# Kernel optimization log

Hardware: AMD Instinct MI355X
Metric: run time of the kernel (lower is better)

## Reference

```python
import jax, jax.numpy as jnp
import numpy as np

N_NODES = 50000
N_EDGES = 1_600_000
D = 128


def setup_inputs() -> dict:
    key = jax.random.key(0)
    k1, k2, k3 = jax.random.split(key, 3)
    x = jax.random.normal(k1, (N_NODES, D), dtype=jnp.float32)
    edge_index = jax.random.randint(k2, (2, N_EDGES), 0, N_NODES, dtype=jnp.int64)
    W = jax.random.normal(k3, (D, D), dtype=jnp.float32) / np.sqrt(D)
    b = jnp.zeros((D,), dtype=jnp.float32)
    return {"x": x, "edge_index": edge_index, "W": W, "b": b}


def _sgconv(x, src, dst, W, b, n):
    # gcn_norm with self-loops: D^{-1/2} (A + I) D^{-1/2}
    loop = jnp.arange(n, dtype=src.dtype)
    src = jnp.concatenate([src, loop])
    dst = jnp.concatenate([dst, loop])
    ones = jnp.ones(src.shape[0], dtype=x.dtype)
    deg = jax.ops.segment_sum(ones, dst, num_segments=n)  # in-degree incl. self-loop
    dinv = jnp.where(deg > 0, jax.lax.rsqrt(deg), jnp.zeros_like(deg))
    norm = dinv[src] * dinv[dst]                      # [E+N]
    msg = x[src] * norm[:, None]                      # gather + scale, [E+N, D]
    agg = jax.ops.segment_sum(msg, dst, num_segments=n)  # scatter-add, [N, D]
    return agg @ W.T + b                              # SGConv linear (K=1)


def reference(x, edge_index, W, b):
    n = x.shape[0]
    h = _sgconv(x, edge_index[0], edge_index[1], W, b, n)
    return x + jax.nn.relu(h)
```

## Files before the change

kernel.cpp:

```cpp
#include <hip/hip_runtime.h>
#include <hip/hip_fp16.h>

#define D 128
#define BSHIFT 6
#define BSIZE 64
#define NBMAX 1024
#define BCAP 3072
#define PREP_BLOCKS 256
#define OVF_CAP 65536
#define GB_THREADS 1024

using half8 = __attribute__((ext_vector_type(8))) _Float16;
using float4v = __attribute__((ext_vector_type(4))) float;
using floatx2 = __attribute__((ext_vector_type(2))) float;

__global__ __launch_bounds__(256) void prep_kernel(const int* __restrict__ src,
                                                   const int* __restrict__ dst,
                                                   int* __restrict__ bucket_cnt,
                                                   int* __restrict__ pairs,
                                                   int* __restrict__ ovfA_cnt,
                                                   int2* __restrict__ ovfA,
                                                   int E, int NB) {
    __shared__ int sbase[NBMAX];
    __shared__ int cur[NBMAX];
    const int t = threadIdx.x;
    for (int b = t; b < NB; b += 256) { sbase[b] = 0; cur[b] = 0; }
    __syncthreads();

    int chunk = (((E + (int)gridDim.x - 1) / (int)gridDim.x) + 3) & ~3;
    int start = blockIdx.x * chunk;
    int end = min(start + chunk, E);

    for (int i = start + 4 * t; i < end; i += 4 * 256) {
        if (i + 3 < end) {
            int4 v = *(const int4*)&dst[i];
            atomicAdd(&sbase[v.x >> BSHIFT], 1);
            atomicAdd(&sbase[v.y >> BSHIFT], 1);
            atomicAdd(&sbase[v.z >> BSHIFT], 1);
            atomicAdd(&sbase[v.w >> BSHIFT], 1);
        } else {
            for (int j = i; j < end; ++j) atomicAdd(&sbase[dst[j] >> BSHIFT], 1);
        }
    }
    __syncthreads();

    for (int b = t; b < NB; b += 256) {
        int h = sbase[b];
        sbase[b] = h ? atomicAdd(&bucket_cnt[b], h) : 0;
    }
    __syncthreads();

    auto place = [&](int dd, int ss) {
        int b = dd >> BSHIFT;
        int p = sbase[b] + atomicAdd(&cur[b], 1);
        if (p < BCAP) {
            pairs[(size_t)b * BCAP + p] = (ss << BSHIFT) | (dd & (BSIZE - 1));
        } else {
            int q = atomicAdd(ovfA_cnt, 1);
            if (q < OVF_CAP) ovfA[q] = make_int2(dd, ss);
        }
    };

    for (int i = start + 4 * t; i < end; i += 4 * 256) {
        if (i + 3 < end) {
            int4 dv = *(const int4*)&dst[i];
            int4 sv = *(const int4*)&src[i];
            place(dv.x, sv.x);
            place(dv.y, sv.y);
            place(dv.z, sv.z);
            place(dv.w, sv.w);
        } else {
            for (int j = i; j < end; ++j) place(dst[j], src[j]);
        }
    }
}

__global__ __launch_bounds__(256) void xw_kernel(const float* __restrict__ x,
                                                 const float* __restrict__ W,
                                                 const int* __restrict__ pairs,
                                                 const int* __restrict__ bucket_cnt,
                                                 const int* __restrict__ ovfA_cnt,
                                                 const int2* __restrict__ ovfA,
                                                 unsigned char* __restrict__ xw, int N) {
    __shared__ _Float16 Bf[128 * 128];
    __shared__ int degX[BSIZE];
    const int t = threadIdx.x;
    const int b = blockIdx.x;
    if (t < BSIZE) degX[t] = 0;
    __syncthreads();

    {
        int cnt = min(bucket_cnt[b], BCAP);
        const int* pp = pairs + (size_t)b * BCAP;
        for (int i = t; i < cnt; i += 256) atomicAdd(&degX[pp[i] & (BSIZE - 1)], 1);
        int na = *ovfA_cnt;
        if (na > 0) {
            if (na > OVF_CAP) na = OVF_CAP;
            for (int k = t; k < na; k += 256) {
                int dd = ovfA[k].x;
                if ((dd >> BSHIFT) == b) atomicAdd(&degX[dd & (BSIZE - 1)], 1);
            }
        }
    }

    {
        int n = t >> 1;
        int jt = n >> 4, nlo = n & 15;
        int kbase = (t & 1) * 64;
#pragma unroll
        for (int o = 0; o < 8; ++o) {
            int k0 = kbase + o * 8;
            float4 f0 = *(const float4*)&W[n * 128 + k0];
            float4 f1 = *(const float4*)&W[n * 128 + k0 + 4];
            int kt = k0 >> 5, quad = (k0 >> 3) & 3;
            half8 h;
            h[0] = (_Float16)f0.x; h[1] = (_Float16)f0.y;
            h[2] = (_Float16)f0.z; h[3] = (_Float16)f0.w;
            h[4] = (_Float16)f1.x; h[5] = (_Float16)f1.y;
            h[6] = (_Float16)f1.z; h[7] = (_Float16)f1.w;
            *(half8*)&Bf[(size_t)(((kt * 8 + jt) * 4 + quad) * 16 + nlo) * 8] = h;
        }
    }
    __syncthreads();

    const int wave = t >> 6, lane = t & 63;
    const int quad = lane >> 4, nlo = lane & 15;
    const int r0 = b * 64 + wave * 16;
    const int rA = r0 + nlo;
    const int rAc = (rA < N) ? rA : (N - 1);
    const float dv = rsqrtf((float)degX[rAc - b * 64] + 1.0f);

    float4v acc[8];
#pragma unroll
    for (int j = 0; j < 8; ++j) acc[j] = (float4v){0.f, 0.f, 0.f, 0.f};

#pragma unroll
    for (int kt = 0; kt < 4; ++kt) {
        const float* xp = x + (size_t)rAc * D + kt * 32 + quad * 8;
        float4 a0 = *(const float4*)xp;
        float4 a1 = *(const float4*)(xp + 4);
        half8 va;
        va[0] = (_Float16)(a0.x * dv); va[1] = (_Float16)(a0.y * dv);
        va[2] = (_Float16)(a0.z * dv); va[3] = (_Float16)(a0.w * dv);
        va[4] = (_Float16)(a1.x * dv); va[5] = (_Float16)(a1.y * dv);
        va[6] = (_Float16)(a1.z * dv); va[7] = (_Float16)(a1.w * dv);
#pragma unroll
        for (int jt = 0; jt < 8; ++jt) {
            half8 vb = *(half8*)&Bf[(size_t)((kt * 8 + jt) * 64 + lane) * 8];
            acc[jt] = __builtin_amdgcn_mfma_f32_16x16x32_f16(va, vb, acc[jt], 0, 0, 0);
        }
    }

#pragma unroll
    for (int reg = 0; reg < 4; ++reg) {
        int row = r0 + quad * 4 + reg;
        if (row < N) {
            int u0 = __builtin_amdgcn_cvt_pk_fp8_f32(acc[0][reg], acc[1][reg], 0, false);
            u0 = __builtin_amdgcn_cvt_pk_fp8_f32(acc[2][reg], acc[3][reg], u0, true);
            int u1 = __builtin_amdgcn_cvt_pk_fp8_f32(acc[4][reg], acc[5][reg], 0, false);
            u1 = __builtin_amdgcn_cvt_pk_fp8_f32(acc[6][reg], acc[7][reg], u1, true);
            *(uint2*)(xw + (size_t)row * 128 + nlo * 8) = make_uint2((unsigned)u0, (unsigned)u1);
        }
    }
}

__global__ __launch_bounds__(GB_THREADS) void gatherB_kernel(
    const float* __restrict__ x, const unsigned char* __restrict__ xw,
    const int* __restrict__ pairs, const int* __restrict__ bucket_cnt,
    const float* __restrict__ bias, const int* __restrict__ ovfA_cnt,
    const int2* __restrict__ ovfA, float* __restrict__ out, int N) {
    __shared__ int lds_src[BCAP];
    __shared__ int degL[BSIZE], offs[BSIZE], cur[BSIZE], spillc[BSIZE];
    const int b = blockIdx.x;
    const int t = threadIdx.x;
    if (t < BSIZE) { degL[t] = 0; cur[t] = 0; spillc[t] = 0; }
    __syncthreads();
    const int cnt = min(bucket_cnt[b], BCAP);
    int na = *ovfA_cnt;
    if (na > OVF_CAP) na = OVF_CAP;

    int my_w[3], my_n = 0;
    for (int i = t; i < cnt; i += GB_THREADS) {
        int w = pairs[(size_t)b * BCAP + i];
        my_w[my_n++] = w;
        atomicAdd(&degL[w & (BSIZE - 1)], 1);
    }
    if (na > 0) {
        for (int k = t; k < na; k += GB_THREADS) {
            int dd = ovfA[k].x;
            if ((dd >> BSHIFT) == b) atomicAdd(&spillc[dd & (BSIZE - 1)], 1);
        }
    }
    __syncthreads();

    if (t < BSIZE) {
        int v = degL[t];
        int s = v;
#pragma unroll
        for (int o = 1; o < 64; o <<= 1) {
            int u = __shfl_up(s, o, 64);
            if (t >= o) s += u;
        }
        offs[t] = s - v;
    }
    __syncthreads();

    for (int k = 0; k < my_n; ++k) {
        int w = my_w[k];
        int dl = w & (BSIZE - 1);
        int p = atomicAdd(&cur[dl], 1);
        lds_src[offs[dl] + p] = w >> BSHIFT;
    }
    __syncthreads();

    const int wave = t >> 6, lane = t & 63;
    const int half = lane >> 5, c31 = lane & 31;
    const unsigned int* xw32 = (const unsigned int*)xw;

    int col[4];
    float bcol[4];
#pragma unroll
    for (int k = 0; k < 4; ++k) {
        int s = 4 * c31 + k;
        col[k] = ((s & 7) << 4) + (s >> 3);
        bcol[k] = bias[col[k]];
    }

    for (int q = 0; q < 4; ++q) {
        int dl = wave * 4 + q;
        int node = b * BSIZE + dl;
        if (node >= N) break;
        int start = offs[dl];
        int end = start + degL[dl];
        float dvd = rsqrtf((float)(degL[dl] + spillc[dl]) + 1.0f);
        size_t noff = (size_t)node * D;

        float a0 = 0.f, a1 = 0.f, a2 = 0.f, a3 = 0.f;

        int e = start;
        for (; e + 7 < end; e += 8) {
            int r0 = lds_src[e + 0 + half], r1 = lds_src[e + 2 + half];
            int r2 = lds_src[e + 4 + half], r3 = lds_src[e + 6 + half];
            unsigned int w0 = xw32[(size_t)r0 * 32 + c31];
            unsigned int w1 = xw32[(size_t)r1 * 32 + c31];
            unsigned int w2 = xw32[(size_t)r2 * 32 + c31];
            unsigned int w3 = xw32[(size_t)r3 * 32 + c31];
            floatx2 l0 = __builtin_amdgcn_cvt_pk_f32_fp8((int)w0, false);
            floatx2 h0 = __builtin_amdgcn_cvt_pk_f32_fp8((int)w0, true);
            floatx2 l1 = __builtin_amdgcn_cvt_pk_f32_fp8((int)w1, false);
            floatx2 h1 = __builtin_amdgcn_cvt_pk_f32_fp8((int)w1, true);
            floatx2 l2 = __builtin_amdgcn_cvt_pk_f32_fp8((int)w2, false);
            floatx2 h2 = __builtin_amdgcn_cvt_pk_f32_fp8((int)w2, true);
            floatx2 l3 = __builtin_amdgcn_cvt_pk_f32_fp8((int)w3, false);
            floatx2 h3 = __builtin_amdgcn_cvt_pk_f32_fp8((int)w3, true);
            a0 += (l0.x + l1.x) + (l2.x + l3.x);
            a1 += (l0.y + l1.y) + (l2.y + l3.y);
            a2 += (h0.x + h1.x) + (h2.x + h3.x);
            a3 += (h0.y + h1.y) + (h2.y + h3.y);
        }
        for (; e + 1 < end; e += 2) {
            int r = lds_src[e + half];
            unsigned int w = xw32[(size_t)r * 32 + c31];
            floatx2 lo = __builtin_amdgcn_cvt_pk_f32_fp8((int)w, false);
            floatx2 hi = __builtin_amdgcn_cvt_pk_f32_fp8((int)w, true);
            a0 += lo.x; a1 += lo.y; a2 += hi.x; a3 += hi.y;
        }
        if (e < end && half == 0) {
            int r = lds_src[e];
            unsigned int w = xw32[(size_t)r * 32 + c31];
            floatx2 lo = __builtin_amdgcn_cvt_pk_f32_fp8((int)w, false);
            floatx2 hi = __builtin_amdgcn_cvt_pk_f32_fp8((int)w, true);
            a0 += lo.x; a1 += lo.y; a2 += hi.x; a3 += hi.y;
        }

        a0 += __shfl_xor(a0, 32);
        a1 += __shfl_xor(a1, 32);
        a2 += __shfl_xor(a2, 32);
        a3 += __shfl_xor(a3, 32);

        float s0 = half ? a2 : a0;
        float s1 = half ? a3 : a1;
        {
            unsigned int ws = xw32[(size_t)node * 32 + c31] >> (half * 16);
            floatx2 sv = __builtin_amdgcn_cvt_pk_f32_fp8((int)ws, false);
            s0 += sv.x; s1 += sv.y;
            if (na > 0) {
                for (int k = 0; k < na; ++k) {
                    int2 pr = ovfA[k];
                    if (pr.x == node) {
                        unsigned int w = xw32[(size_t)pr.y * 32 + c31] >> (half * 16);
                        floatx2 v2 = __builtin_amdgcn_cvt_pk_f32_fp8((int)w, false);
                        s0 += v2.x; s1 += v2.y;
                    }
                }
            }
        }
        int c0 = col[2 * half], c1 = col[2 * half + 1];
        float h0 = s0 * dvd + bcol[2 * half];
        float h1 = s1 * dvd + bcol[2 * half + 1];
        out[noff + c0] = x[noff + c0] + (h0 > 0.f ? h0 : 0.f);
        out[noff + c1] = x[noff + c1] + (h1 > 0.f ? h1 : 0.f);
    }
}

extern "C" void kernel_launch(void* const* d_in, const int* in_sizes, int n_in,
                              void* d_out, int out_size, void* d_ws, size_t ws_size,
                              hipStream_t stream) {
    const float* x = (const float*)d_in[0];
    const int* ei = (const int*)d_in[1];
    const float* W = (const float*)d_in[2];
    const float* bias = (const float*)d_in[3];
    float* out = (float*)d_out;

    const int N = in_sizes[0] / D;
    const int E = in_sizes[1] / 2;
    const int* src = ei;
    const int* dst = ei + E;
    const int NB = (N + BSIZE - 1) / BSIZE;

    char* p = (char*)d_ws;
    int* pairs = (int*)p;            p += (size_t)NB * BCAP * sizeof(int);
    unsigned char* xw = (unsigned char*)p; p += (size_t)N * 128;
    int* bucket_cnt = (int*)p;       p += (size_t)NBMAX * sizeof(int);
    int* ovfA_cnt = (int*)p;         p += 16;
    int2* ovfA = (int2*)p;           p += (size_t)OVF_CAP * sizeof(int2);

    hipMemsetAsync(bucket_cnt, 0, (size_t)NBMAX * sizeof(int) + 16, stream);

    prep_kernel<<<PREP_BLOCKS, 256, 0, stream>>>(src, dst, bucket_cnt, pairs,
                                                 ovfA_cnt, ovfA, E, NB);
    xw_kernel<<<NB, 256, 0, stream>>>(x, W, pairs, bucket_cnt, ovfA_cnt, ovfA, xw, N);
    gatherB_kernel<<<NB, GB_THREADS, 0, stream>>>(x, xw, pairs, bucket_cnt,
                                                  bias, ovfA_cnt, ovfA, out, N);
}
```

Measured before the change: 156.9 us.

## Compute per-node degrees globally in prep and widen gather unroll

The prep kernel now also does a global atomicAdd per edge into a per-node degree array, so the xw and gather kernels no longer rebuild degrees from bucket pairs and scan the overflow list. The prep grid changes from a fixed 256 blocks to about 391 blocks that each cover 4096 edges, with the edge data held in registers between the histogram pass and the placement pass. The gather loop gets a 16-edge unrolled path to keep more loads in flight. The cost is 1.6M global atomics on a 200KB array and a larger memset.

After: 213.4 us. +36.0%, slower.

```diff
diff --git a/kernel.cpp b/kernel.cpp
--- a/kernel.cpp
+++ b/kernel.cpp
@@ -6,7 +6,7 @@
 #define BSIZE 64
 #define NBMAX 1024
 #define BCAP 3072
-#define PREP_BLOCKS 256
+#define PREP_ITERS 4
 #define OVF_CAP 65536
 #define GB_THREADS 1024
 
@@ -17,6 +17,7 @@
 __global__ __launch_bounds__(256) void prep_kernel(const int* __restrict__ src,
                                                    const int* __restrict__ dst,
                                                    int* __restrict__ bucket_cnt,
+                                                   int* __restrict__ deg,
                                                    int* __restrict__ pairs,
                                                    int* __restrict__ ovfA_cnt,
                                                    int2* __restrict__ ovfA,
@@ -27,21 +28,25 @@
     for (int b = t; b < NB; b += 256) { sbase[b] = 0; cur[b] = 0; }
     __syncthreads();
 
-    int chunk = (((E + (int)gridDim.x - 1) / (int)gridDim.x) + 3) & ~3;
-    int start = blockIdx.x * chunk;
-    int end = min(start + chunk, E);
-
-    for (int i = start + 4 * t; i < end; i += 4 * 256) {
-        if (i + 3 < end) {
-            int4 v = *(const int4*)&dst[i];
-            atomicAdd(&sbase[v.x >> BSHIFT], 1);
-            atomicAdd(&sbase[v.y >> BSHIFT], 1);
-            atomicAdd(&sbase[v.z >> BSHIFT], 1);
-            atomicAdd(&sbase[v.w >> BSHIFT], 1);
-        } else {
-            for (int j = i; j < end; ++j) atomicAdd(&sbase[dst[j] >> BSHIFT], 1);
-        }
-    }
+    const int E4 = E & ~3;
+    const int sbeg = blockIdx.x * (PREP_ITERS * 1024);
+    const int send = min(sbeg + PREP_ITERS * 1024, E4);
+    const int base = sbeg + 4 * t;
+
+    int4 dv[PREP_ITERS], sv[PREP_ITERS];
+#pragma unroll
+    for (int it = 0; it < PREP_ITERS; ++it) {
+        int i = base + it * 1024;
+        if (i < send) {
+            dv[it] = *(const int4*)&dst[i];
+            sv[it] = *(const int4*)&src[i];
+            atomicAdd(&sbase[dv[it].x >> BSHIFT], 1);
+            atomicAdd(&sbase[dv[it].y >> BSHIFT], 1);
+            atomicAdd(&sbase[dv[it].z >> BSHIFT], 1);
+            atomicAdd(&sbase[dv[it].w >> BSHIFT], 1);
+        }
+    }
+    if (blockIdx.x == 0 && t < (E & 3)) atomicAdd(&sbase[dst[E4 + t] >> BSHIFT], 1);
     __syncthreads();
 
     for (int b = t; b < NB; b += 256) {
@@ -51,6 +56,7 @@
     __syncthreads();
 
     auto place = [&](int dd, int ss) {
+        atomicAdd(&deg[dd], 1);
         int b = dd >> BSHIFT;
         int p = sbase[b] + atomicAdd(&cur[b], 1);
         if (p < BCAP) {
@@ -61,47 +67,29 @@
         }
     };
 
-    for (int i = start + 4 * t; i < end; i += 4 * 256) {
-        if (i + 3 < end) {
-            int4 dv = *(const int4*)&dst[i];
-            int4 sv = *(const int4*)&src[i];
-            place(dv.x, sv.x);
-            place(dv.y, sv.y);
-            place(dv.z, sv.z);
-            place(dv.w, sv.w);
-        } else {
-            for (int j = i; j < end; ++j) place(dst[j], src[j]);
-        }
+#pragma unroll
+    for (int it = 0; it < PREP_ITERS; ++it) {
+        int i = base + it * 1024;
+        if (i < send) {
+            place(dv[it].x, sv[it].x);
+            place(dv[it].y, sv[it].y);
+            place(dv[it].z, sv[it].z);
+            place(dv[it].w, sv[it].w);
+        }
+    }
+    if (blockIdx.x == 0 && t < (E & 3)) {
+        int j = E4 + t;
+        place(dst[j], src[j]);
     }
 }
 
 __global__ __launch_bounds__(256) void xw_kernel(const float* __restrict__ x,
                                                  const float* __restrict__ W,
-                                                 const int* __restrict__ pairs,
-                                                 const int* __restrict__ bucket_cnt,
-                                                 const int* __restrict__ ovfA_cnt,
-                                                 const int2* __restrict__ ovfA,
+                                                 const int* __restrict__ deg,
                                                  unsigned char* __restrict__ xw, int N) {
     __shared__ _Float16 Bf[128 * 128];
-    __shared__ int degX[BSIZE];
     const int t = threadIdx.x;
     const int b = blockIdx.x;
-    if (t < BSIZE) degX[t] = 0;
-    __syncthreads();
-
-    {
-        int cnt = min(bucket_cnt[b], BCAP);
-        const int* pp = pairs + (size_t)b * BCAP;
-        for (int i = t; i < cnt; i += 256) atomicAdd(&degX[pp[i] & (BSIZE - 1)], 1);
-        int na = *ovfA_cnt;
-        if (na > 0) {
-            if (na > OVF_CAP) na = OVF_CAP;
-            for (int k = t; k < na; k += 256) {
-                int dd = ovfA[k].x;
-                if ((dd >> BSHIFT) == b) atomicAdd(&degX[dd & (BSIZE - 1)], 1);
-            }
-        }
-    }
 
     {
         int n = t >> 1;
@@ -128,7 +116,7 @@
     const int r0 = b * 64 + wave * 16;
     const int rA = r0 + nlo;
     const int rAc = (rA < N) ? rA : (N - 1);
-    const float dv = rsqrtf((float)degX[rAc - b * 64] + 1.0f);
+    const float dv = rsqrtf((float)deg[rAc] + 1.0f);
 
     float4v acc[8];
 #pragma unroll
@@ -167,13 +155,14 @@
 __global__ __launch_bounds__(GB_THREADS) void gatherB_kernel(
     const float* __restrict__ x, const unsigned char* __restrict__ xw,
     const int* __restrict__ pairs, const int* __restrict__ bucket_cnt,
+    const int* __restrict__ deg,
     const float* __restrict__ bias, const int* __restrict__ ovfA_cnt,
     const int2* __restrict__ ovfA, float* __restrict__ out, int N) {
     __shared__ int lds_src[BCAP];
-    __shared__ int degL[BSIZE], offs[BSIZE], cur[BSIZE], spillc[BSIZE];
+    __shared__ int degL[BSIZE], offs[BSIZE], cur[BSIZE];
     const int b = blockIdx.x;
     const int t = threadIdx.x;
-    if (t < BSIZE) { degL[t] = 0; cur[t] = 0; spillc[t] = 0; }
+    if (t < BSIZE) { degL[t] = 0; cur[t] = 0; }
     __syncthreads();
     const int cnt = min(bucket_cnt[b], BCAP);
     int na = *ovfA_cnt;
@@ -184,12 +173,6 @@
         int w = pairs[(size_t)b * BCAP + i];
         my_w[my_n++] = w;
         atomicAdd(&degL[w & (BSIZE - 1)], 1);
-    }
-    if (na > 0) {
-        for (int k = t; k < na; k += GB_THREADS) {
-            int dd = ovfA[k].x;
-            if ((dd >> BSHIFT) == b) atomicAdd(&spillc[dd & (BSIZE - 1)], 1);
-        }
     }
     __syncthreads();
 
@@ -232,12 +215,26 @@
         if (node >= N) break;
         int start = offs[dl];
         int end = start + degL[dl];
-        float dvd = rsqrtf((float)(degL[dl] + spillc[dl]) + 1.0f);
+        float dvd = rsqrtf((float)deg[node] + 1.0f);
         size_t noff = (size_t)node * D;
 
         float a0 = 0.f, a1 = 0.f, a2 = 0.f, a3 = 0.f;
 
         int e = start;
+        for (; e + 15 < end; e += 16) {
+            int rr[8];
+#pragma unroll
+            for (int u = 0; u < 8; ++u) rr[u] = lds_src[e + 2 * u + half];
+            unsigned int wv[8];
+#pragma unroll
+            for (int u = 0; u < 8; ++u) wv[u] = xw32[(size_t)rr[u] * 32 + c31];
+#pragma unroll
+            for (int u = 0; u < 8; ++u) {
+                floatx2 lo = __builtin_amdgcn_cvt_pk_f32_fp8((int)wv[u], false);
+                floatx2 hi = __builtin_amdgcn_cvt_pk_f32_fp8((int)wv[u], true);
+                a0 += lo.x; a1 += lo.y; a2 += hi.x; a3 += hi.y;
+            }
+        }
         for (; e + 7 < end; e += 8) {
             int r0 = lds_src[e + 0 + half], r1 = lds_src[e + 2 + half];
             int r2 = lds_src[e + 4 + half], r3 = lds_src[e + 6 + half];
@@ -323,13 +320,17 @@
     unsigned char* xw = (unsigned char*)p; p += (size_t)N * 128;
     int* bucket_cnt = (int*)p;       p += (size_t)NBMAX * sizeof(int);
     int* ovfA_cnt = (int*)p;         p += 16;
+    int* deg = (int*)p;              p += (size_t)NBMAX * BSIZE * sizeof(int);
     int2* ovfA = (int2*)p;           p += (size_t)OVF_CAP * sizeof(int2);
 
-    hipMemsetAsync(bucket_cnt, 0, (size_t)NBMAX * sizeof(int) + 16, stream);
-
-    prep_kernel<<<PREP_BLOCKS, 256, 0, stream>>>(src, dst, bucket_cnt, pairs,
-                                                 ovfA_cnt, ovfA, E, NB);
-    xw_kernel<<<NB, 256, 0, stream>>>(x, W, pairs, bucket_cnt, ovfA_cnt, ovfA, xw, N);
-    gatherB_kernel<<<NB, GB_THREADS, 0, stream>>>(x, xw, pairs, bucket_cnt,
+    hipMemsetAsync(bucket_cnt, 0,
+                   (size_t)NBMAX * sizeof(int) + 16 + (size_t)NBMAX * BSIZE * sizeof(int),
+                   stream);
+
+    const int nPrep = (E + PREP_ITERS * 4096 / PREP_ITERS - 1) / 4096;
+    prep_kernel<<<nPrep, 256, 0, stream>>>(src, dst, bucket_cnt, deg, pairs,
+                                           ovfA_cnt, ovfA, E, NB);
+    xw_kernel<<<NB, 256, 0, stream>>>(x, W, deg, xw, N);
+    gatherB_kernel<<<NB, GB_THREADS, 0, stream>>>(x, xw, pairs, bucket_cnt, deg,
                                                   bias, ovfA_cnt, ovfA, out, N);
 }
```

## Pad bucket counters, double prep blocks, deepen gather unroll to 16 edges

Applied to the files above, without the earlier changes.

Each bucket counter now sits on its own 64-byte line, so the global atomics from prep blocks no longer contend on shared lines. The number of prep blocks doubles to spread the binning over more workgroups. The gather kernel's pair-loading loop becomes three fixed predicated loads instead of a dynamic register array, and a 16-edge unrolled gather loop puts more independent fp8 loads in flight. The costs are more atomics on the per-bucket counters, a larger memset, and higher register pressure.

Measured after the change: 175.8 us. 1.12x slower.

```diff
diff --git a/kernel.cpp b/kernel.cpp
--- a/kernel.cpp
+++ b/kernel.cpp
@@ -6,7 +6,8 @@
 #define BSIZE 64
 #define NBMAX 1024
 #define BCAP 3072
-#define PREP_BLOCKS 256
+#define CPAD 16
+#define PREP_BLOCKS 512
 #define OVF_CAP 65536
 #define GB_THREADS 1024
 
@@ -46,7 +47,7 @@
 
     for (int b = t; b < NB; b += 256) {
         int h = sbase[b];
-        sbase[b] = h ? atomicAdd(&bucket_cnt[b], h) : 0;
+        sbase[b] = h ? atomicAdd(&bucket_cnt[b * CPAD], h) : 0;
     }
     __syncthreads();
 
@@ -90,7 +91,7 @@
     __syncthreads();
 
     {
-        int cnt = min(bucket_cnt[b], BCAP);
+        int cnt = min(bucket_cnt[b * CPAD], BCAP);
         const int* pp = pairs + (size_t)b * BCAP;
         for (int i = t; i < cnt; i += 256) atomicAdd(&degX[pp[i] & (BSIZE - 1)], 1);
         int na = *ovfA_cnt;
@@ -175,16 +176,16 @@
     const int t = threadIdx.x;
     if (t < BSIZE) { degL[t] = 0; cur[t] = 0; spillc[t] = 0; }
     __syncthreads();
-    const int cnt = min(bucket_cnt[b], BCAP);
+    const int cnt = min(bucket_cnt[b * CPAD], BCAP);
     int na = *ovfA_cnt;
     if (na > OVF_CAP) na = OVF_CAP;
 
-    int my_w[3], my_n = 0;
-    for (int i = t; i < cnt; i += GB_THREADS) {
-        int w = pairs[(size_t)b * BCAP + i];
-        my_w[my_n++] = w;
-        atomicAdd(&degL[w & (BSIZE - 1)], 1);
-    }
+    const int* slab = pairs + (size_t)b * BCAP;
+    int w0 = 0, w1 = 0, w2 = 0;
+    const bool p0 = t < cnt, p1 = t + 1024 < cnt, p2 = t + 2048 < cnt;
+    if (p0) { w0 = slab[t];        atomicAdd(&degL[w0 & (BSIZE - 1)], 1); }
+    if (p1) { w1 = slab[t + 1024]; atomicAdd(&degL[w1 & (BSIZE - 1)], 1); }
+    if (p2) { w2 = slab[t + 2048]; atomicAdd(&degL[w2 & (BSIZE - 1)], 1); }
     if (na > 0) {
         for (int k = t; k < na; k += GB_THREADS) {
             int dd = ovfA[k].x;
@@ -205,12 +206,9 @@
     }
     __syncthreads();
 
-    for (int k = 0; k < my_n; ++k) {
-        int w = my_w[k];
-        int dl = w & (BSIZE - 1);
-        int p = atomicAdd(&cur[dl], 1);
-        lds_src[offs[dl] + p] = w >> BSHIFT;
-    }
+    if (p0) { int dl = w0 & (BSIZE - 1); lds_src[offs[dl] + atomicAdd(&cur[dl], 1)] = w0 >> BSHIFT; }
+    if (p1) { int dl = w1 & (BSIZE - 1); lds_src[offs[dl] + atomicAdd(&cur[dl], 1)] = w1 >> BSHIFT; }
+    if (p2) { int dl = w2 & (BSIZE - 1); lds_src[offs[dl] + atomicAdd(&cur[dl], 1)] = w2 >> BSHIFT; }
     __syncthreads();
 
     const int wave = t >> 6, lane = t & 63;
@@ -238,21 +236,35 @@
         float a0 = 0.f, a1 = 0.f, a2 = 0.f, a3 = 0.f;
 
         int e = start;
+        for (; e + 15 < end; e += 16) {
+            int rr[8];
+#pragma unroll
+            for (int u = 0; u < 8; ++u) rr[u] = lds_src[e + 2 * u + half];
+            unsigned int wv[8];
+#pragma unroll
+            for (int u = 0; u < 8; ++u) wv[u] = xw32[(size_t)rr[u] * 32 + c31];
+#pragma unroll
+            for (int u = 0; u < 8; ++u) {
+                floatx2 lo = __builtin_amdgcn_cvt_pk_f32_fp8((int)wv[u], false);
+                floatx2 hi = __builtin_amdgcn_cvt_pk_f32_fp8((int)wv[u], true);
+                a0 += lo.x; a1 += lo.y; a2 += hi.x; a3 += hi.y;
+            }
+        }
         for (; e + 7 < end; e += 8) {
             int r0 = lds_src[e + 0 + half], r1 = lds_src[e + 2 + half];
             int r2 = lds_src[e + 4 + half], r3 = lds_src[e + 6 + half];
-            unsigned int w0 = xw32[(size_t)r0 * 32 + c31];
-            unsigned int w1 = xw32[(size_t)r1 * 32 + c31];
-            unsigned int w2 = xw32[(size_t)r2 * 32 + c31];
-            unsigned int w3 = xw32[(size_t)r3 * 32 + c31];
-            floatx2 l0 = __builtin_amdgcn_cvt_pk_f32_fp8((int)w0, false);
-            floatx2 h0 = __builtin_amdgcn_cvt_pk_f32_fp8((int)w0, true);
-            floatx2 l1 = __builtin_amdgcn_cvt_pk_f32_fp8((int)w1, false);
-            floatx2 h1 = __builtin_amdgcn_cvt_pk_f32_fp8((int)w1, true);
-            floatx2 l2 = __builtin_amdgcn_cvt_pk_f32_fp8((int)w2, false);
-            floatx2 h2 = __builtin_amdgcn_cvt_pk_f32_fp8((int)w2, true);
-            floatx2 l3 = __builtin_amdgcn_cvt_pk_f32_fp8((int)w3, false);
-            floatx2 h3 = __builtin_amdgcn_cvt_pk_f32_fp8((int)w3, true);
+            unsigned int q0 = xw32[(size_t)r0 * 32 + c31];
+            unsigned int q1 = xw32[(size_t)r1 * 32 + c31];
+            unsigned int q2 = xw32[(size_t)r2 * 32 + c31];
+            unsigned int q3 = xw32[(size_t)r3 * 32 + c31];
+            floatx2 l0 = __builtin_amdgcn_cvt_pk_f32_fp8((int)q0, false);
+            floatx2 h0 = __builtin_amdgcn_cvt_pk_f32_fp8((int)q0, true);
+            floatx2 l1 = __builtin_amdgcn_cvt_pk_f32_fp8((int)q1, false);
+            floatx2 h1 = __builtin_amdgcn_cvt_pk_f32_fp8((int)q1, true);
+            floatx2 l2 = __builtin_amdgcn_cvt_pk_f32_fp8((int)q2, false);
+            floatx2 h2 = __builtin_amdgcn_cvt_pk_f32_fp8((int)q2, true);
+            floatx2 l3 = __builtin_amdgcn_cvt_pk_f32_fp8((int)q3, false);
+            floatx2 h3 = __builtin_amdgcn_cvt_pk_f32_fp8((int)q3, true);
             a0 += (l0.x + l1.x) + (l2.x + l3.x);
             a1 += (l0.y + l1.y) + (l2.y + l3.y);
             a2 += (h0.x + h1.x) + (h2.x + h3.x);
@@ -321,11 +333,11 @@
     char* p = (char*)d_ws;
     int* pairs = (int*)p;            p += (size_t)NB * BCAP * sizeof(int);
     unsigned char* xw = (unsigned char*)p; p += (size_t)N * 128;
-    int* bucket_cnt = (int*)p;       p += (size_t)NBMAX * sizeof(int);
+    int* bucket_cnt = (int*)p;       p += (size_t)NBMAX * CPAD * sizeof(int);
     int* ovfA_cnt = (int*)p;         p += 16;
     int2* ovfA = (int2*)p;           p += (size_t)OVF_CAP * sizeof(int2);
 
-    hipMemsetAsync(bucket_cnt, 0, (size_t)NBMAX * sizeof(int) + 16, stream);
+    hipMemsetAsync(bucket_cnt, 0, (size_t)NBMAX * CPAD * sizeof(int) + 16, stream);
 
     prep_kernel<<<PREP_BLOCKS, 256, 0, stream>>>(src, dst, bucket_cnt, pairs,
                                                  ovfA_cnt, ovfA, E, NB);
```
